# Kernel optimization log

Measured on AMD Instinct MI355X. Metric: run time of the kernel, lower is better.

## Reference

```python
import jax, jax.numpy as jnp
import numpy as np

N = 512       # building thermal nodes (state dim)
M = 9         # inputs: [Tout(t), Q_1..Q_8]
T = 20000     # RK4 grid points
DT = 30.0     # seconds per step (as in docstring example)
N_DATA = 2000 # outside-temperature breakpoints for interp


def setup_inputs() -> dict:
    key = jax.random.key(0)
    kA, kB, kQ, kT, kiv = jax.random.split(key, 5)
    # Stable continuous-time system: spectral radius ~5e-3 -> |lambda*dt| ~ 0.2
    A = (jax.random.normal(kA, (N, N), jnp.float32) * 1e-4
         - 5e-3 * jnp.eye(N, dtype=jnp.float32))
    B = jax.random.normal(kB, (N, M), jnp.float32) * 1e-3
    Q = jax.random.uniform(kQ, (M - 1,), jnp.float32) * 100.0  # heat gains
    t_eval = jnp.arange(T, dtype=jnp.float32) * DT
    # interp1d replacement: sorted breakpoints + diurnal temperature signal
    Tout_t = jnp.linspace(0.0, T * DT, N_DATA).astype(jnp.float32)
    Tout_v = (15.0 + 10.0 * jnp.sin(2.0 * jnp.pi * Tout_t / 86400.0)
              + jax.random.normal(kT, (N_DATA,), jnp.float32))
    iv = 20.0 + jax.random.normal(kiv, (N,), jnp.float32)
    return {"A": A, "B": B, "Q": Q, "Tout_t": Tout_t, "Tout_v": Tout_v,
            "iv": iv, "t_eval": t_eval}


def reference(A, B, Q, Tout_t, Tout_v, iv, t_eval):
    """RK4 (torchdiffeq 3/8-rule fixed-grid) integration of dx/dt = A@x + B@u(t)."""

    def f(t, x):
        Tout = jnp.interp(t, Tout_t, Tout_v)          # on-device interp1d
        u = jnp.concatenate([Tout[None], Q])          # [M]
        return A @ x + B @ u                          # [N]

    def step(x, td):
        t, dt = td
        k1 = f(t, x)
        k2 = f(t + dt / 3.0, x + dt * k1 / 3.0)
        k3 = f(t + dt * 2.0 / 3.0, x + dt * (k2 - k1 / 3.0))
        k4 = f(t + dt, x + dt * (k1 - k2 + k3))
        x_new = x + dt * (k1 + 3.0 * (k2 + k3) + k4) / 8.0
        return x_new, x_new

    ts = t_eval[:-1]
    dts = jnp.diff(t_eval)
    _, xs = jax.lax.scan(step, iv, (ts, dts))         # [T-1, N]
    return jnp.concatenate([iv[None, :], xs], axis=0)  # [T, N]
```

## Files before the change

### kernel.cpp

```cpp
#include <hip/hip_runtime.h>

#define TT    20000
#define CCH   2500
#define RROWS 2501
#define NDATA 2000
#define MSZ   262144

typedef unsigned short u16;
typedef unsigned int   u32;
using f32x4 = __attribute__((ext_vector_type(4))) float;
using s16x8 = __attribute__((ext_vector_type(8))) short;

static constexpr size_t OFF_HT  = 0;
static constexpr size_t OFF_H2T = (size_t)MSZ;
static constexpr size_t OFF_MP  = 2*(size_t)MSZ;
static constexpr size_t OFF_SQ  = 10*(size_t)MSZ;
static constexpr size_t OFF_VEC = 12*(size_t)MSZ;
static constexpr size_t OFF_FJ  = OFF_VEC + 4096;
static constexpr size_t OFF_AL  = OFF_FJ + 163840;
static constexpr size_t OFF_SA  = OFF_AL + 102400;
static constexpr size_t OFF_SB  = OFF_SA + (size_t)RROWS*512;

__device__ __forceinline__ u16 f2bf(float f) {
    u32 u = __float_as_uint(f);
    u += 0x7fff + ((u >> 16) & 1);
    return (u16)(u >> 16);
}

#define MICRO_FMA(a, b) do { \
  acc0.x += (a).x*(b).x; acc0.y += (a).x*(b).y; acc0.z += (a).x*(b).z; acc0.w += (a).x*(b).w; \
  acc1.x += (a).y*(b).x; acc1.y += (a).y*(b).y; acc1.z += (a).y*(b).z; acc1.w += (a).y*(b).w; \
  acc2.x += (a).z*(b).x; acc2.y += (a).z*(b).y; acc2.z += (a).z*(b).z; acc2.w += (a).z*(b).w; \
  acc3.x += (a).w*(b).x; acc3.y += (a).w*(b).y; acc3.z += (a).w*(b).z; acc3.w += (a).w*(b).w; \
} while (0)

#define DECL_GEMM_VARS() \
    int t = threadIdx.x; \
    int tx = t & 15, ty = t >> 4; \
    int ar = t & 63, ak4 = (t >> 6) * 4; \
    int bk = t >> 4, bc4 = (t & 15) * 4; \
    float4 acc0 = {0,0,0,0}, acc1 = {0,0,0,0}, acc2 = {0,0,0,0}, acc3 = {0,0,0,0}; \
    (void)tx; (void)ty; (void)ar; (void)ak4; (void)bk; (void)bc4

#define GEMM_CORE_DB(LOADA, LOADB) \
    { float4 ra = LOADA(0); float4 rbv = LOADB(0); \
    As[0][ak4+0][ar]=ra.x; As[0][ak4+1][ar]=ra.y; As[0][ak4+2][ar]=ra.z; As[0][ak4+3][ar]=ra.w; \
    *(float4*)&Bs[0][bk][bc4] = rbv; \
    for (int kt = 1; kt <= 32; kt++) { \
        __syncthreads(); \
        const int cur = (kt - 1) & 1; \
        if (kt < 32) { ra = LOADA(kt); rbv = LOADB(kt); } \
        _Pragma("unroll") \
        for (int kk = 0; kk < 16; kk++) { \
            float4 a = *(const float4*)&As[cur][kk][ty*4]; \
            float4 b = *(const float4*)&Bs[cur][kk][tx*4]; \
            MICRO_FMA(a, b); \
        } \
        if (kt < 32) { const int nb = kt & 1; \
            As[nb][ak4+0][ar]=ra.x; As[nb][ak4+1][ar]=ra.y; As[nb][ak4+2][ar]=ra.z; As[nb][ak4+3][ar]=ra.w; \
            *(float4*)&Bs[nb][bk][bc4] = rbv; } \
    } }

__device__ __forceinline__ void pow_tile(const float* __restrict__ Ap,
                                         const float* __restrict__ Bp,
                                         float* __restrict__ Zp, int idx) {
    __shared__ float As[2][16][68], Bs[2][16][68];
    DECL_GEMM_VARS();
    int rb = (idx >> 3) * 64, cb = (idx & 7) * 64;
#define LA(kt) (*(const float4*)&Ap[(size_t)(rb+ar)*512 + (kt)*16 + ak4])
#define LB(kt) (*(const float4*)&Bp[(size_t)((kt)*16+bk)*512 + cb + bc4])
    GEMM_CORE_DB(LA, LB)
#undef LA
#undef LB
    size_t zb = (size_t)(rb + ty*4)*512 + cb + tx*4;
    *(float4*)&Zp[zb]        = acc0;
    *(float4*)&Zp[zb + 512]  = acc1;
    *(float4*)&Zp[zb + 1024] = acc2;
    *(float4*)&Zp[zb + 1536] = acc3;
}

__device__ __forceinline__ void matvecT128(const float* __restrict__ MT,
                                           const float* __restrict__ x,
                                           float* __restrict__ y, int rb,
                                           const float* __restrict__ gc,
                                           const float* __restrict__ gu1,
                                           const float* __restrict__ gu2) {
    __shared__ float xs[512];
    __shared__ float red2[2][128];
    int t = threadIdx.x;
    xs[t] = x[t]; xs[t + 256] = x[t + 256];
    __syncthreads();
    int rl = t & 127, h = t >> 7;
    size_t col = (size_t)rb + rl;
    float acc = 0.f;
    int k0 = h << 8;
    #pragma unroll 4
    for (int k = k0; k < k0 + 256; k++) acc += MT[(size_t)k*512 + col] * xs[k];
    red2[h][rl] = acc;
    __syncthreads();
    if (t < 128) {
        float s = red2[0][t] + red2[1][t];
        int r = rb + t;
        if (gc) y[r] = 30.f * (gc[r] + 0.5f*gu1[r] + (1.f/6.f)*gu2[r] + (1.f/24.f)*s);
        else    y[r] = s;
    }
}

__device__ __forceinline__ float interp1(float tt, const float* __restrict__ xp,
                                         const float* __restrict__ fp) {
    if (tt <= xp[0]) return fp[0];
    if (tt >= xp[NDATA-1]) return fp[NDATA-1];
    int lo = 0, hi = NDATA - 1;
    while (hi - lo > 1) { int mid = (lo + hi) >> 1; if (xp[mid] <= tt) lo = mid; else hi = mid; }
    float x0 = xp[lo], x1 = xp[lo+1];
    return fp[lo] + (fp[lo+1] - fp[lo]) * (tt - x0) / (x1 - x0);
}

__global__ __launch_bounds__(256) void k_setup(const float* __restrict__ A,
        const float* __restrict__ B, const float* __restrict__ Q,
        const float* __restrict__ te, const float* __restrict__ Tt,
        const float* __restrict__ Tv, const float* __restrict__ iv,
        float* __restrict__ HT, float* __restrict__ vec, float* __restrict__ AL,
        float* __restrict__ out, float* __restrict__ SA) {
    int bx = blockIdx.x, t = threadIdx.x;
    if (bx < 256) {
        __shared__ float Ts[32][33];
        int tr = bx >> 4, tc = bx & 15;
        int rl = t >> 3, cl4 = (t & 7) * 4;
        float4 a = *(const float4*)&A[(size_t)(tr*32 + rl)*512 + tc*32 + cl4];
        Ts[rl][cl4+0] = 30.f*a.x; Ts[rl][cl4+1] = 30.f*a.y;
        Ts[rl][cl4+2] = 30.f*a.z; Ts[rl][cl4+3] = 30.f*a.w;
        __syncthreads();
        float4 o;
        o.x = Ts[cl4+0][rl]; o.y = Ts[cl4+1][rl]; o.z = Ts[cl4+2][rl]; o.w = Ts[cl4+3][rl];
        *(float4*)&HT[(size_t)(tc*32 + rl)*512 + tr*32 + cl4] = o;
    } else if (bx == 256) {
        for (int i = t; i < 512; i += 256) {
            float v = B[i*9];
            float c = 0.f;
            #pragma unroll
            for (int j = 0; j < 8; j++) c += B[i*9 + 1 + j] * Q[j];
            vec[i] = v;
            vec[2560 + i] = c;
        }
    } else if (bx == 257) {
        for (int i = t; i < 512; i += 256) { out[i] = iv[i]; SA[i] = iv[i]; }
    } else {
        int n = (bx - 258) * 256 + t;
        if (n >= TT) return;
        float* a = AL + (size_t)n * 5;
        if (n == TT - 1) { a[0]=a[1]=a[2]=a[3]=a[4]=0.f; return; }
        float tt = te[n];
        float T1 = interp1(tt, Tt, Tv);
        float T2 = interp1(tt + 10.f, Tt, Tv);
        float T3 = interp1(tt + 20.f, Tt, Tv);
        float T4 = interp1(tt + 30.f, Tt, Tv);
        a[0] = 3.75f * (T1 + 3.f*T2 + 3.f*T3 + T4);
        a[1] = 3.75f * (T1 + 2.f*T2 + T3);
        a[2] = 3.75f * (T1*(1.f/3.f) + T2);
        a[3] = 1.25f * T1;
        a[4] = 1.f;
    }
}

__global__ __launch_bounds__(256) void k_h2kv(const float* __restrict__ HT,
                                              float* __restrict__ H2T,
                                              float* __restrict__ vec) {
    int bx = blockIdx.x;
    if (bx < 64) { pow_tile(HT, HT, H2T, bx); return; }
    int sub = bx - 64, which = sub >> 2, rb = (sub & 3) * 128;
    if (which == 0) matvecT128(HT, vec,        vec + 512,  rb, 0, 0, 0);
    else            matvecT128(HT, vec + 2560, vec + 3072, rb, 0, 0, 0);
}

__global__ __launch_bounds__(256) void k_m1kv(const float* __restrict__ HT,
                                              const float* __restrict__ H2T,
                                              float* __restrict__ M1T,
                                              float* __restrict__ vec) {
    int bx = blockIdx.x;
    if (bx < 64) {
        __shared__ float As[2][16][68], Bs[2][16][68];
        DECL_GEMM_VARS();
        int rb = (bx >> 3) * 64, cb = (bx & 7) * 64;
#define LA(kt) ({ size_t off = (size_t)(rb+ar)*512 + (kt)*16 + ak4; \
        float4 h  = *(const float4*)&HT[off]; \
        float4 h2 = *(const float4*)&H2T[off]; \
        float4 r_; \
        r_.x = h.x*(1.f/6.f) + h2.x*(1.f/24.f); r_.y = h.y*(1.f/6.f) + h2.y*(1.f/24.f); \
        r_.z = h.z*(1.f/6.f) + h2.z*(1.f/24.f); r_.w = h.w*(1.f/6.f) + h2.w*(1.f/24.f); \
        int dd = (rb+ar) - ((kt)*16 + ak4); \
        if (dd >= 0 && dd < 4) (&r_.x)[dd] += 0.5f; \
        r_; })
#define LB(kt) (*(const float4*)&H2T[(size_t)((kt)*16+bk)*512 + cb + bc4])
        GEMM_CORE_DB(LA, LB)
#undef LA
#undef LB
        int col = cb + tx*4;
        #pragma unroll
        for (int i = 0; i < 4; i++) {
            int r = rb + ty*4 + i;
            float4 h = *(const float4*)&HT[(size_t)r*512 + col];
            float4* ac = (i==0) ? &acc0 : (i==1) ? &acc1 : (i==2) ? &acc2 : &acc3;
            ac->x += h.x + (r == col+0 ? 1.f : 0.f);
            ac->y += h.y + (r == col+1 ? 1.f : 0.f);
            ac->z += h.z + (r == col+2 ? 1.f : 0.f);
            ac->w += h.w + (r == col+3 ? 1.f : 0.f);
            *(float4*)&M1T[(size_t)r*512 + col] = *ac;
        }
        return;
    }
    int sub = bx - 64, which = sub >> 2, rb = (sub & 3) * 128;
    if (which == 0) matvecT128(HT, vec + 512,  vec + 1024, rb, 0, 0, 0);
    else            matvecT128(HT, vec + 3072, vec + 3584, rb, 0, 0, 0);
}

__global__ __launch_bounds__(256) void k_m2kv(const float* __restrict__ M1T,
                                              float* __restrict__ M2T,
                                              const float* __restrict__ HT,
                                              float* __restrict__ vec) {
    int bx = blockIdx.x;
    if (bx < 64) { pow_tile(M1T, M1T, M2T, bx); return; }
    int sub = bx - 64, which = sub >> 2, rb = (sub & 3) * 128;
    if (which == 0) matvecT128(HT, vec + 1024, vec + 1536, rb, 0, 0, 0);
    else matvecT128(HT, vec + 3584, vec + 2048, rb,
                    vec + 2560, vec + 3072, vec + 3584);
}

__global__ __launch_bounds__(256) void k_pow(const float* __restrict__ A,
                                             const float* __restrict__ B0,
                                             float* __restrict__ Z0) {
    int sel = blockIdx.x >> 6;
    pow_tile(A, B0 + (size_t)sel*MSZ, Z0 + (size_t)sel*MSZ, blockIdx.x & 63);
}

__global__ __launch_bounds__(256) void k_wgen_sq(const float* __restrict__ vec,
                                                 const float* __restrict__ MP,
                                                 float* __restrict__ FJ,
                                                 const float* __restrict__ P,
                                                 float* __restrict__ Pout) {
    int bx = blockIdx.x;
    if (bx >= 64) { pow_tile(P, P, Pout, bx - 64); return; }
    int d = bx >> 3, cb = (bx & 7) * 64;
    int t = threadIdx.x;
    if (d == 0) {
        for (int idx = t; idx < 320; idx += 256) {
            int r = idx >> 6, c = idx & 63;
            float s = vec[(size_t)r*512 + cb + c];
            #pragma unroll
            for (int i = 0; i < 8; i++)
                FJ[((size_t)i*40 + i*5 + r)*512 + cb + c] = s;
        }
        for (int j = 0; j < 7; j++)
            for (int i = j + 1; i < 8; i++)
                for (int idx = t; idx < 320; idx += 256) {
                    int r = idx >> 6, c = idx & 63;
                    FJ[((size_t)j*40 + i*5 + r)*512 + cb + c] = 0.f;
                }
        return;
    }
    __shared__ float Ws[5][512];
    __shared__ float red4[4][5][64];
    const float* Mj = MP + (size_t)(d - 1)*MSZ;
    for (int e = t; e < 2560; e += 256) Ws[e >> 9][e & 511] = vec[e];
    __syncthreads();
    int col = t & 63, kq = t >> 6, k0 = kq * 128;
    float acc[5] = {0.f, 0.f, 0.f, 0.f, 0.f};
    #pragma unroll 4
    for (int k = k0; k < k0 + 128; k++) {
        float m = Mj[(size_t)k*512 + cb + col];
        acc[0] += Ws[0][k]*m; acc[1] += Ws[1][k]*m; acc[2] += Ws[2][k]*m;
        acc[3] += Ws[3][k]*m; acc[4] += Ws[4][k]*m;
    }
    #pragma unroll
    for (int r = 0; r < 5; r++) red4[kq][r][col] = acc[r];
    __syncthreads();
    for (int idx = t; idx < 320; idx += 256) {
        int r = idx >> 6, c = idx & 63;
        float s = red4[0][r][c] + red4[1][r][c] + red4[2][r][c] + red4[3][r][c];
        for (int i = 0; i + d < 8; i++)
            FJ[((size_t)(i + d)*40 + i*5 + r)*512 + cb + c] = s;
    }
}

__global__ __launch_bounds__(256) void k_e40_sq(const float* __restrict__ AL,
                                                const float* __restrict__ FJ,
                                                float* __restrict__ SA1,
                                                const float* __restrict__ P,
                                                float* __restrict__ Pout) {
    int bx = blockIdx.x;
    if (bx >= 320) { pow_tile(P, P, Pout, bx - 320); return; }
    const float* GT = FJ + (size_t)7*40*512;
    int kb = (bx >> 3) * 64, cb = (bx & 7) * 64;
    __shared__ float Ah[64][41], Bsv[40][68];
    int t = threadIdx.x;
    int tx = t & 15, ty = t >> 4;
    #pragma unroll
    for (int m = 0; m < 10; m++) {
        int e = t + 256*m;
        int row = e / 40, q = e - 40*row;
        float v = 0.f;
        if (kb + row < CCH) v = AL[(size_t)(kb + row)*40 + q];
        Ah[row][q] = v;
        int fq = e >> 6, fc = e & 63;
        Bsv[fq][fc] = GT[(size_t)fq*512 + cb + fc];
    }
    __syncthreads();
    float4 acc0 = {0,0,0,0}, acc1 = {0,0,0,0}, acc2 = {0,0,0,0}, acc3 = {0,0,0,0};
    #pragma unroll 8
    for (int q = 0; q < 40; q++) {
        float4 b = *(const float4*)&Bsv[q][tx*4];
        float a0 = Ah[ty*4+0][q], a1 = Ah[ty*4+1][q];
        float a2 = Ah[ty*4+2][q], a3 = Ah[ty*4+3][q];
        acc0.x += a0*b.x; acc0.y += a0*b.y; acc0.z += a0*b.z; acc0.w += a0*b.w;
        acc1.x += a1*b.x; acc1.y += a1*b.y; acc1.z += a1*b.z; acc1.w += a1*b.w;
        acc2.x += a2*b.x; acc2.y += a2*b.y; acc2.z += a2*b.z; acc2.w += a2*b.w;
        acc3.x += a3*b.x; acc3.y += a3*b.y; acc3.z += a3*b.z; acc3.w += a3*b.w;
    }
    int col = cb + tx*4;
    #pragma unroll
    for (int i = 0; i < 4; i++) {
        int k = kb + ty*4 + i;
        if (k < CCH) {
            float4 a = (i==0) ? acc0 : (i==1) ? acc1 : (i==2) ? acc2 : acc3;
            *(float4*)&SA1[(size_t)k*512 + col] = a;
        }
    }
}

__global__ __launch_bounds__(256) void k_scan_sq(const float* __restrict__ Ain,
                                                 float* __restrict__ Aout,
                                                 const float* __restrict__ QT, int shift,
                                                 const float* __restrict__ P,
                                                 float* __restrict__ Pout) {
    int bx = blockIdx.x;
    if (bx >= 320) { pow_tile(P, P, Pout, bx - 320); return; }
    __shared__ float As[2][16][68], Bs[2][16][68];
    DECL_GEMM_VARS();
    int kb = (bx >> 3) * 64, cb = (bx & 7) * 64;
    int xr = kb + ar - shift;
    bool aval = (xr >= 0) && (kb + ar < RROWS);
#define LA(kt) ({ float4 z = {0,0,0,0}; \
        if (aval) z = *(const float4*)&Ain[(size_t)xr*512 + (kt)*16 + ak4]; z; })
#define LB(kt) (*(const float4*)&QT[(size_t)((kt)*16+bk)*512 + cb + bc4])
    GEMM_CORE_DB(LA, LB)
#undef LA
#undef LB
    int col = cb + tx*4;
    #pragma unroll
    for (int i = 0; i < 4; i++) {
        int krow = kb + ty*4 + i;
        if (krow < RROWS) {
            float4 own = *(const float4*)&Ain[(size_t)krow*512 + col];
            float4 a = (i==0) ? acc0 : (i==1) ? acc1 : (i==2) ? acc2 : acc3;
            float4 res = {own.x + a.x, own.y + a.y, own.z + a.z, own.w + a.w};
            *(float4*)&Aout[(size_t)krow*512 + col] = res;
        }
    }
}

__global__ __launch_bounds__(256) void k_mprep(const float* __restrict__ MPin,
                                               u16* __restrict__ Mbf) {
    int j = blockIdx.x >> 6, tile = blockIdx.x & 63;
    int kb = (tile >> 3) * 64, cb = (tile & 7) * 64;
    const float* MT = MPin + (size_t)j * MSZ;
    __shared__ float Ts[64][65];
    int t = threadIdx.x;
    int lr = t >> 4, lc = (t & 15) * 4;
    #pragma unroll
    for (int p = 0; p < 4; p++) {
        float4 v = *(const float4*)&MT[(size_t)(kb + p*16 + lr)*512 + cb + lc];
        Ts[p*16+lr][lc+0] = v.x; Ts[p*16+lr][lc+1] = v.y;
        Ts[p*16+lr][lc+2] = v.z; Ts[p*16+lr][lc+3] = v.w;
    }
    __syncthreads();
    int r = t >> 2, c16 = (t & 3) * 16;
    u32 pk[8];
    #pragma unroll
    for (int i = 0; i < 8; i++) {
        u32 a = f2bf(Ts[c16 + 2*i][r]);
        u32 b = f2bf(Ts[c16 + 2*i + 1][r]);
        pk[i] = a | (b << 16);
    }
    u16* dst = Mbf + (size_t)j*MSZ + (size_t)(cb + r)*512 + kb + c16;
    *(uint4*)dst       = make_uint4(pk[0], pk[1], pk[2], pk[3]);
    *(uint4*)(dst + 8) = make_uint4(pk[4], pk[5], pk[6], pk[7]);
}

__global__ __launch_bounds__(256) void k_final(const float* __restrict__ SS,
                                               const u16* __restrict__ Mbf,
                                               const float* __restrict__ AL,
                                               const float* __restrict__ FJ,
                                               float* __restrict__ out) {
    __shared__ float smem[8448];
    u16* Asu = (u16*)smem;
    u16* Bsu = (u16*)(smem + 2560);
    int t = threadIdx.x;
    int lane = t & 63, w = t >> 6;
    int lo16 = lane & 15, hi = lane >> 4;
    int j = blockIdx.x >> 3;
    int cb = (blockIdx.x & 7) * 64;
    int kb = blockIdx.y * 128;
    const u16* Bm = Mbf + (size_t)j * MSZ;

    f32x4 acc[2][4];
    #pragma unroll
    for (int m = 0; m < 2; m++)
        #pragma unroll
        for (int n = 0; n < 4; n++) acc[m][n] = 0.f;

    int s_row = t >> 3;
    int s_k4  = (t & 7) * 4;
    int b_row = t >> 2;
    int b_k8  = (t & 3) * 8;

    for (int kt = 0; kt < 16; kt++) {
        __syncthreads();
        #pragma unroll
        for (int p = 0; p < 4; p++) {
            int r = p*32 + s_row;
            float4 v = {0.f, 0.f, 0.f, 0.f};
            if (kb + r < CCH) v = *(const float4*)&SS[(size_t)(kb+r)*512 + kt*32 + s_k4];
            uint2 pk;
            pk.x = (u32)f2bf(v.x) | ((u32)f2bf(v.y) << 16);
            pk.y = (u32)f2bf(v.z) | ((u32)f2bf(v.w) << 16);
            *(uint2*)&Asu[r*40 + s_k4] = pk;
        }
        {
            uint4 v = *(const uint4*)&Bm[(size_t)(cb + b_row)*512 + kt*32 + b_k8];
            *(uint4*)&Bsu[b_row*40 + b_k8] = v;
        }
        __syncthreads();
        s16x8 a0 = *(const s16x8*)&Asu[(w*32      + lo16)*40 + hi*8];
        s16x8 a1 = *(const s16x8*)&Asu[(w*32 + 16 + lo16)*40 + hi*8];
        #pragma unroll
        for (int n = 0; n < 4; n++) {
            s16x8 b = *(const s16x8*)&Bsu[(n*16 + lo16)*40 + hi*8];
            acc[0][n] = __builtin_amdgcn_mfma_f32_16x16x32_bf16(a0, b, acc[0][n], 0, 0, 0);
            acc[1][n] = __builtin_amdgcn_mfma_f32_16x16x32_bf16(a1, b, acc[1][n], 0, 0, 0);
        }
    }
    __syncthreads();
    float (*Ah)[44] = (float(*)[44])smem;
    float (*Fs)[44] = (float(*)[44])(smem + 5632);
    {
        int row = t >> 1, half = t & 1;
        #pragma unroll
        for (int i = 0; i < 5; i++) {
            float4 v = {0.f, 0.f, 0.f, 0.f};
            if (kb + row < CCH) v = *(const float4*)&AL[(size_t)(kb+row)*40 + half*20 + i*4];
            *(float4*)&Ah[row][half*20 + i*4] = v;
        }
        #pragma unroll
        for (int m = 0; m < 10; m++) {
            int e = t + 256*m;
            int q = e >> 6, c = e & 63;
            Fs[c][q] = FJ[(size_t)j*40*512 + (size_t)q*512 + cb + c];
        }
    }
    __syncthreads();
    #pragma unroll
    for (int cq = 0; cq < 10; cq++) {
        float4 bv[4];
        #pragma unroll
        for (int n = 0; n < 4; n++) bv[n] = *(const float4*)&Fs[n*16 + lo16][cq*4];
        #pragma unroll
        for (int m = 0; m < 2; m++) {
            #pragma unroll
            for (int r = 0; r < 4; r++) {
                float4 av = *(const float4*)&Ah[w*32 + m*16 + hi*4 + r][cq*4];
                #pragma unroll
                for (int n = 0; n < 4; n++) {
                    acc[m][n][r] += av.x*bv[n].x + av.y*bv[n].y + av.z*bv[n].z + av.w*bv[n].w;
                }
            }
        }
    }
    #pragma unroll
    for (int m = 0; m < 2; m++) {
        #pragma unroll
        for (int r = 0; r < 4; r++) {
            int k = kb + w*32 + m*16 + hi*4 + r;
            int n_out = 8*k + j + 1;
            if (k < CCH && n_out < TT) {
                #pragma unroll
                for (int n = 0; n < 4; n++)
                    out[(size_t)n_out*512 + cb + n*16 + lo16] = acc[m][n][r];
            }
        }
    }
}

extern "C" void kernel_launch(void* const* d_in, const int* in_sizes, int n_in,
                              void* d_out, int out_size, void* d_ws, size_t ws_size,
                              hipStream_t stream) {
    const float* A  = (const float*)d_in[0];
    const float* B  = (const float*)d_in[1];
    const float* Q  = (const float*)d_in[2];
    const float* Tt = (const float*)d_in[3];
    const float* Tv = (const float*)d_in[4];
    const float* iv = (const float*)d_in[5];
    const float* te = (const float*)d_in[6];
    float* out = (float*)d_out;
    float* w = (float*)d_ws;

    float* HT  = w + OFF_HT;
    float* H2T = w + OFF_H2T;
    float* MP  = w + OFF_MP;
    float* SQ  = w + OFF_SQ;
    float* vec = w + OFF_VEC;
    float* FJ  = w + OFF_FJ;
    float* AL  = w + OFF_AL;
    float* SA  = w + OFF_SA;
    float* SB  = w + OFF_SB;

    float* M16 = H2T;
    float* M32 = HT;
    float* M64 = SQ;
    float* M8  = MP + 7*(size_t)MSZ;
    u16*   Mbf = (u16*)SB;

    k_setup<<<337, 256, 0, stream>>>(A, B, Q, te, Tt, Tv, iv, HT, vec, AL, out, SA);
    k_h2kv<<<72, 256, 0, stream>>>(HT, H2T, vec);
    k_m1kv<<<72, 256, 0, stream>>>(HT, H2T, MP, vec);
    k_m2kv<<<72, 256, 0, stream>>>(MP, MP + MSZ, HT, vec);
    k_pow<<<128, 256, 0, stream>>>(MP + MSZ, MP, MP + 2*(size_t)MSZ);
    k_pow<<<256, 256, 0, stream>>>(MP + 3*(size_t)MSZ, MP, MP + 4*(size_t)MSZ);
    k_wgen_sq<<<128, 256, 0, stream>>>(vec, MP, FJ, M8, M16);
    k_e40_sq<<<384, 256, 0, stream>>>(AL, FJ, SA + 512, M16, M32);
    k_scan_sq<<<384, 256, 0, stream>>>(SA, SB, M8,  1, M32, M64);
    k_scan_sq<<<320, 256, 0, stream>>>(SB, SA, M16, 2, nullptr, nullptr);
    k_scan_sq<<<320, 256, 0, stream>>>(SA, SB, M32, 4, nullptr, nullptr);
    k_scan_sq<<<320, 256, 0, stream>>>(SB, SA, M64, 8, nullptr, nullptr);
    k_mprep<<<512, 256, 0, stream>>>(MP, Mbf);
    k_final<<<dim3(64, 20), 256, 0, stream>>>(SA, Mbf, AL, FJ, out);
}
```

Measured before the change: 553.4 us.

## Retile final GEMM to full-width column blocks with register prefetch and transposed FJ

The final output kernel now assigns each block 32 time rows across all 512 columns rather than 128 rows by 64 columns. This loads each A (state) tile once and streams the whole bf16 M matrix through LDS, with global loads for the next k-step prefetched into registers during the MFMA work. FJ is pre-transposed inside k_mprep via extra blocks so the epilogue reads it straight from global memory instead of staging it through LDS. The trade-off is more M traffic per block, a larger LDS footprint and more accumulators per thread, which could limit occupancy.

```diff
diff --git a/kernel.cpp b/kernel.cpp
--- a/kernel.cpp
+++ b/kernel.cpp
@@ -359,12 +359,25 @@
 }
 
 __global__ __launch_bounds__(256) void k_mprep(const float* __restrict__ MPin,
-                                               u16* __restrict__ Mbf) {
-    int j = blockIdx.x >> 6, tile = blockIdx.x & 63;
+                                               u16* __restrict__ Mbf,
+                                               const float* __restrict__ FJ,
+                                               float* __restrict__ FJT) {
+    int bx = blockIdx.x;
+    int t = threadIdx.x;
+    if (bx >= 512) {
+        int bx2 = bx - 512;
+        int j = bx2 >> 1, half = bx2 & 1;
+        int col = half*256 + t;
+        const float* Fb = FJ + (size_t)j*40*512 + col;
+        float* Ft = FJT + (size_t)j*512*40 + (size_t)col*40;
+        #pragma unroll 8
+        for (int q = 0; q < 40; q++) Ft[q] = Fb[(size_t)q*512];
+        return;
+    }
+    int j = bx >> 6, tile = bx & 63;
     int kb = (tile >> 3) * 64, cb = (tile & 7) * 64;
     const float* MT = MPin + (size_t)j * MSZ;
     __shared__ float Ts[64][65];
-    int t = threadIdx.x;
     int lr = t >> 4, lc = (t & 15) * 4;
     #pragma unroll
     for (int p = 0; p < 4; p++) {
@@ -386,92 +399,95 @@
     *(uint4*)(dst + 8) = make_uint4(pk[4], pk[5], pk[6], pk[7]);
 }
 
-__global__ __launch_bounds__(256) void k_final(const float* __restrict__ SS,
+__global__ __launch_bounds__(256, 2) void k_final(const float* __restrict__ SS,
                                                const u16* __restrict__ Mbf,
                                                const float* __restrict__ AL,
-                                               const float* __restrict__ FJ,
+                                               const float* __restrict__ FJT,
                                                float* __restrict__ out) {
-    __shared__ float smem[8448];
-    u16* Asu = (u16*)smem;
-    u16* Bsu = (u16*)(smem + 2560);
+    __shared__ u16 Bsu[512*36];
+    __shared__ u16 Asu[32*36];
+    __shared__ float Ah[32][40];
     int t = threadIdx.x;
     int lane = t & 63, w = t >> 6;
     int lo16 = lane & 15, hi = lane >> 4;
-    int j = blockIdx.x >> 3;
-    int cb = (blockIdx.x & 7) * 64;
-    int kb = blockIdx.y * 128;
-    const u16* Bm = Mbf + (size_t)j * MSZ;
-
-    f32x4 acc[2][4];
+    int j = blockIdx.x;
+    int kb = blockIdx.y * 32;
+
+    int b_r  = t >> 2;
+    int b_k8 = (t & 3) * 8;
+    int a_r  = t >> 3;
+    int a_c4 = (t & 7) * 4;
+    const u16* Bb = Mbf + (size_t)j*MSZ;
+    const float* Ab = SS + (size_t)(kb + a_r)*512 + a_c4;
+    const bool aval = (kb + a_r) < CCH;
+
+    f32x4 acc[2][8];
     #pragma unroll
     for (int m = 0; m < 2; m++)
         #pragma unroll
-        for (int n = 0; n < 4; n++) acc[m][n] = 0.f;
-
-    int s_row = t >> 3;
-    int s_k4  = (t & 7) * 4;
-    int b_row = t >> 2;
-    int b_k8  = (t & 3) * 8;
-
+        for (int n = 0; n < 8; n++) acc[m][n] = 0.f;
+
+    uint4 pb[8]; float4 pa;
+#define PREFETCH(kt) do { \
+    _Pragma("unroll") \
+    for (int p = 0; p < 8; p++) \
+        pb[p] = *(const uint4*)&Bb[(size_t)(p*64 + b_r)*512 + (kt)*32 + b_k8]; \
+    const float4 z4_ = {0.f,0.f,0.f,0.f}; \
+    pa = aval ? *(const float4*)&Ab[(kt)*32] : z4_; \
+} while (0)
+#define STORE_LDS() do { \
+    _Pragma("unroll") \
+    for (int p = 0; p < 8; p++) \
+        *(uint4*)&Bsu[(p*64 + b_r)*36 + b_k8] = pb[p]; \
+    uint2 pk_; \
+    pk_.x = (u32)f2bf(pa.x) | ((u32)f2bf(pa.y) << 16); \
+    pk_.y = (u32)f2bf(pa.z) | ((u32)f2bf(pa.w) << 16); \
+    *(uint2*)&Asu[a_r*36 + a_c4] = pk_; \
+} while (0)
+
+    PREFETCH(0);
     for (int kt = 0; kt < 16; kt++) {
         __syncthreads();
+        STORE_LDS();
+        __syncthreads();
+        if (kt < 15) PREFETCH(kt + 1);
+        __builtin_amdgcn_sched_barrier(0);
+        s16x8 fa0 = *(const s16x8*)&Asu[(lo16)*36 + hi*8];
+        s16x8 fa1 = *(const s16x8*)&Asu[(16 + lo16)*36 + hi*8];
         #pragma unroll
-        for (int p = 0; p < 4; p++) {
-            int r = p*32 + s_row;
-            float4 v = {0.f, 0.f, 0.f, 0.f};
-            if (kb + r < CCH) v = *(const float4*)&SS[(size_t)(kb+r)*512 + kt*32 + s_k4];
-            uint2 pk;
-            pk.x = (u32)f2bf(v.x) | ((u32)f2bf(v.y) << 16);
-            pk.y = (u32)f2bf(v.z) | ((u32)f2bf(v.w) << 16);
-            *(uint2*)&Asu[r*40 + s_k4] = pk;
-        }
-        {
-            uint4 v = *(const uint4*)&Bm[(size_t)(cb + b_row)*512 + kt*32 + b_k8];
-            *(uint4*)&Bsu[b_row*40 + b_k8] = v;
-        }
-        __syncthreads();
-        s16x8 a0 = *(const s16x8*)&Asu[(w*32      + lo16)*40 + hi*8];
-        s16x8 a1 = *(const s16x8*)&Asu[(w*32 + 16 + lo16)*40 + hi*8];
+        for (int n = 0; n < 8; n++) {
+            s16x8 fb = *(const s16x8*)&Bsu[((size_t)(w*128 + n*16 + lo16))*36 + hi*8];
+            acc[0][n] = __builtin_amdgcn_mfma_f32_16x16x32_bf16(fa0, fb, acc[0][n], 0, 0, 0);
+            acc[1][n] = __builtin_amdgcn_mfma_f32_16x16x32_bf16(fa1, fb, acc[1][n], 0, 0, 0);
+        }
+    }
+#undef PREFETCH
+#undef STORE_LDS
+
+    __syncthreads();
+    for (int i = t; i < 1280; i += 256) {
+        int row = i / 40, q = i - row*40;
+        float v = 0.f;
+        if (kb + row < CCH) v = AL[(size_t)(kb + row)*40 + q];
+        (&Ah[0][0])[i] = v;
+    }
+    __syncthreads();
+    const float* Ft = FJT + (size_t)j*512*40;
+    int colb = w*128 + lo16;
+    #pragma unroll 2
+    for (int q4 = 0; q4 < 10; q4++) {
+        float4 fv[8];
         #pragma unroll
-        for (int n = 0; n < 4; n++) {
-            s16x8 b = *(const s16x8*)&Bsu[(n*16 + lo16)*40 + hi*8];
-            acc[0][n] = __builtin_amdgcn_mfma_f32_16x16x32_bf16(a0, b, acc[0][n], 0, 0, 0);
-            acc[1][n] = __builtin_amdgcn_mfma_f32_16x16x32_bf16(a1, b, acc[1][n], 0, 0, 0);
-        }
-    }
-    __syncthreads();
-    float (*Ah)[44] = (float(*)[44])smem;
-    float (*Fs)[44] = (float(*)[44])(smem + 5632);
-    {
-        int row = t >> 1, half = t & 1;
-        #pragma unroll
-        for (int i = 0; i < 5; i++) {
-            float4 v = {0.f, 0.f, 0.f, 0.f};
-            if (kb + row < CCH) v = *(const float4*)&AL[(size_t)(kb+row)*40 + half*20 + i*4];
-            *(float4*)&Ah[row][half*20 + i*4] = v;
-        }
-        #pragma unroll
-        for (int m = 0; m < 10; m++) {
-            int e = t + 256*m;
-            int q = e >> 6, c = e & 63;
-            Fs[c][q] = FJ[(size_t)j*40*512 + (size_t)q*512 + cb + c];
-        }
-    }
-    __syncthreads();
-    #pragma unroll
-    for (int cq = 0; cq < 10; cq++) {
-        float4 bv[4];
-        #pragma unroll
-        for (int n = 0; n < 4; n++) bv[n] = *(const float4*)&Fs[n*16 + lo16][cq*4];
+        for (int n = 0; n < 8; n++)
+            fv[n] = *(const float4*)&Ft[(size_t)(colb + n*16)*40 + q4*4];
         #pragma unroll
         for (int m = 0; m < 2; m++) {
             #pragma unroll
             for (int r = 0; r < 4; r++) {
-                float4 av = *(const float4*)&Ah[w*32 + m*16 + hi*4 + r][cq*4];
+                float4 av = *(const float4*)&Ah[m*16 + hi*4 + r][q4*4];
                 #pragma unroll
-                for (int n = 0; n < 4; n++) {
-                    acc[m][n][r] += av.x*bv[n].x + av.y*bv[n].y + av.z*bv[n].z + av.w*bv[n].w;
-                }
+                for (int n = 0; n < 8; n++)
+                    acc[m][n][r] += av.x*fv[n].x + av.y*fv[n].y + av.z*fv[n].z + av.w*fv[n].w;
             }
         }
     }
@@ -479,12 +495,13 @@
     for (int m = 0; m < 2; m++) {
         #pragma unroll
         for (int r = 0; r < 4; r++) {
-            int k = kb + w*32 + m*16 + hi*4 + r;
+            int k = kb + m*16 + hi*4 + r;
             int n_out = 8*k + j + 1;
             if (k < CCH && n_out < TT) {
+                size_t ro = (size_t)n_out*512 + w*128 + lo16;
                 #pragma unroll
-                for (int n = 0; n < 4; n++)
-                    out[(size_t)n_out*512 + cb + n*16 + lo16] = acc[m][n][r];
+                for (int n = 0; n < 8; n++)
+                    out[ro + n*16] = acc[m][n][r];
             }
         }
     }
@@ -518,6 +535,7 @@
     float* M64 = SQ;
     float* M8  = MP + 7*(size_t)MSZ;
     u16*   Mbf = (u16*)SB;
+    float* FJT = SB + 4*(size_t)MSZ;
 
     k_setup<<<337, 256, 0, stream>>>(A, B, Q, te, Tt, Tv, iv, HT, vec, AL, out, SA);
     k_h2kv<<<72, 256, 0, stream>>>(HT, H2T, vec);
@@ -531,6 +549,6 @@
     k_scan_sq<<<320, 256, 0, stream>>>(SB, SA, M16, 2, nullptr, nullptr);
     k_scan_sq<<<320, 256, 0, stream>>>(SA, SB, M32, 4, nullptr, nullptr);
     k_scan_sq<<<320, 256, 0, stream>>>(SB, SA, M64, 8, nullptr, nullptr);
-    k_mprep<<<512, 256, 0, stream>>>(MP, Mbf);
-    k_final<<<dim3(64, 20), 256, 0, stream>>>(SA, Mbf, AL, FJ, out);
-}
+    k_mprep<<<528, 256, 0, stream>>>(MP, Mbf, FJ, FJT);
+    k_final<<<dim3(8, 79), 256, 0, stream>>>(SA, Mbf, AL, FJT, out);
+}
```

Result: faster. 537.0 us (-3.0%).
